# Optimization experiments

Measured on AMD Instinct MI355X. Metric: run time of the kernel, lower is better.

The kernel has to match this reference:

```python
import jax, jax.numpy as jnp
import numpy as np

BATCH, IN, OUT, G = 2048, 512, 512, 8


def setup_inputs() -> dict:
    key = jax.random.key(0)
    k1, k2, k3 = jax.random.split(key, 3)
    x = jax.random.normal(k1, (BATCH, IN), dtype=jnp.float32)
    # spline coefficients, initialized small like normal_(c, 0, 0.001)
    c = jax.random.normal(k2, (G, OUT, IN), dtype=jnp.float32) * 0.001
    # residual weights, xavier-like small init
    w_b = jax.random.normal(k3, (OUT, IN), dtype=jnp.float32) * 0.001
    w_s = jnp.ones((OUT, IN), dtype=jnp.float32)
    # RBF grid centers over [-2, 2] (get_size() == G)
    grid = jnp.arange(G, dtype=jnp.float32) * (4.0 / (G - 1)) - 2.0
    return {"x": x, "c": c, "w_b": w_b, "w_s": w_s, "grid": grid}


def _basis(x, grid):
    # Gaussian RBF basis: [batch, G, in]
    d = x[:, None, :] - grid[None, :, None]
    return jnp.exp(-(d * d))


def reference(x, c, w_b, w_s, grid):
    basis_vals = _basis(x, grid)                      # [b, n=G, i]
    # faithful to th.einsum('bni,aoi->boi', ...): n and a are independently summed
    spline_out = jnp.einsum('bni,aoi->boi', basis_vals, c)  # [b, o, i]
    spline_out = spline_out * w_s[None]
    res_out = jax.nn.silu(x)[:, None, :] * w_b[None]  # [b, o, i]
    return (spline_out + res_out).sum(axis=-1)        # [b, o]
```

## Files before the change

### kernel.cpp

```cpp
#include <hip/hip_runtime.h>

#define BATCH 2048
#define IN    512
#define OUT   512
#define NG    8
#define KTOT  1024

#define TILE_SHORTS 4096
#define NIT 16

typedef __attribute__((ext_vector_type(8))) short bf16x8;
typedef __attribute__((ext_vector_type(4))) float f32x4;

__device__ inline unsigned short f2bf(float f) {
    union { float f; unsigned int u; } v; v.f = f;
    unsigned int r = v.u + 0x7fffu + ((v.u >> 16) & 1u);
    return (unsigned short)(r >> 16);
}

__device__ inline void gload_lds16(const void* g, void* l) {
    __builtin_amdgcn_global_load_lds((const __attribute__((address_space(1))) void*)g,
                                     (__attribute__((address_space(3))) void*)l, 16, 0, 0);
}

__global__ __launch_bounds__(256) void prep_kernel(const float* __restrict__ x,
                                                   const float* __restrict__ c,
                                                   const float* __restrict__ w_b,
                                                   const float* __restrict__ w_s,
                                                   const float* __restrict__ grid,
                                                   unsigned short* __restrict__ A,
                                                   unsigned short* __restrict__ B) {
    int blk = blockIdx.x;
    int tid = threadIdx.x;
    if (blk < 512) {
        int e = (blk * 256 + tid) * 8;
        float g0 = grid[0];
        float dl = grid[1] - g0;
        float d2 = dl * dl;
        float dn[NG];
#pragma unroll
        for (int n = 0; n < NG; ++n) dn[n] = __expf(-d2 * (float)(n * n));
        float4 x0 = *(const float4*)&x[e];
        float4 x1 = *(const float4*)&x[e + 4];
        float xv[8] = {x0.x, x0.y, x0.z, x0.w, x1.x, x1.y, x1.z, x1.w};
        unsigned short sv[8], lv[8];
#pragma unroll
        for (int j = 0; j < 8; ++j) {
            float u  = xv[j] - g0;
            float e1 = __expf(-u * u);
            float q  = __expf(2.f * dl * u);
            float p  = dn[NG - 1];
#pragma unroll
            for (int n = NG - 2; n >= 0; --n) p = p * q + dn[n];
            sv[j] = f2bf(e1 * p);
            lv[j] = f2bf(xv[j] / (1.f + __expf(-xv[j])));
        }
        int b = e >> 9, i = e & 511;
        *(int4*)&A[b * KTOT + i]       = *(int4*)sv;
        *(int4*)&A[b * KTOT + 512 + i] = *(int4*)lv;
    } else {
        int e = ((blk - 512) * 256 + tid) * 8;
        float acc[8] = {};
#pragma unroll
        for (int a = 0; a < NG; ++a) {
            float4 c0 = *(const float4*)&c[(size_t)a * (OUT * IN) + e];
            float4 c1 = *(const float4*)&c[(size_t)a * (OUT * IN) + e + 4];
            acc[0] += c0.x; acc[1] += c0.y; acc[2] += c0.z; acc[3] += c0.w;
            acc[4] += c1.x; acc[5] += c1.y; acc[6] += c1.z; acc[7] += c1.w;
        }
        float4 s0 = *(const float4*)&w_s[e];
        float4 s1 = *(const float4*)&w_s[e + 4];
        float sw[8] = {s0.x, s0.y, s0.z, s0.w, s1.x, s1.y, s1.z, s1.w};
        float4 b0 = *(const float4*)&w_b[e];
        float4 b1 = *(const float4*)&w_b[e + 4];
        float bw[8] = {b0.x, b0.y, b0.z, b0.w, b1.x, b1.y, b1.z, b1.w};
        unsigned short cv[8], bv[8];
#pragma unroll
        for (int j = 0; j < 8; ++j) { cv[j] = f2bf(acc[j] * sw[j]); bv[j] = f2bf(bw[j]); }
        int o = e >> 9, i = e & 511;
        *(int4*)&B[o * KTOT + i]       = *(int4*)cv;
        *(int4*)&B[o * KTOT + 512 + i] = *(int4*)bv;
    }
}

__global__ __launch_bounds__(512) void gemm_kernel(const unsigned short* __restrict__ A,
                                                   const unsigned short* __restrict__ B,
                                                   float* __restrict__ outp) {
    __shared__ short As[3][TILE_SHORTS];
    __shared__ short Bs[3][TILE_SHORTS];

    int tid  = threadIdx.x;
    int lane = tid & 63;
    int w    = tid >> 6;
    int wm   = (w >> 2) & 1;
    int wn   = (w >> 1) & 1;
    int ks   = w & 1;
    int lr   = lane & 15, lg = lane >> 4;

    int bid  = blockIdx.x;
    int mg   = bid & 7;
    int rest = bid >> 3;
    int sub  = rest >> 3;
    int ncol = rest & 7;
    int mt   = mg * 4 + sub;
    int m0   = mt * 64;
    int n0   = ncol * 64;

    int srow = tid >> 3;
    int gsc  = (tid & 7) ^ (srow & 7);
    const unsigned short* a_src = A + (size_t)(m0 + srow) * KTOT + gsc * 8;
    const unsigned short* b_src = B + (size_t)(n0 + srow) * KTOT + gsc * 8;

    int swc  = ((ks * 4 + lg) ^ (lr & 7)) * 8;
    int ra0  = (wm * 32 + lr)      * 64 + swc;
    int ra1  = (wm * 32 + 16 + lr) * 64 + swc;
    int rb0  = (wn * 32 + lr)      * 64 + swc;
    int rb1  = (wn * 32 + 16 + lr) * 64 + swc;

    f32x4 acc00 = {0.f, 0.f, 0.f, 0.f};
    f32x4 acc01 = {0.f, 0.f, 0.f, 0.f};
    f32x4 acc10 = {0.f, 0.f, 0.f, 0.f};
    f32x4 acc11 = {0.f, 0.f, 0.f, 0.f};

#define STAGE(t, buf) do { \
        gload_lds16(a_src + (t) * 64, &As[buf][tid * 8]); \
        gload_lds16(b_src + (t) * 64, &Bs[buf][tid * 8]); \
    } while (0)

    STAGE(0, 0);
    STAGE(1, 1);
    asm volatile("s_waitcnt vmcnt(2)" ::: "memory");
    __builtin_amdgcn_s_barrier();
    __builtin_amdgcn_sched_barrier(0);

#pragma unroll
    for (int it = 0; it < NIT; ++it) {
        int cur = it % 3;
        if (it + 2 < NIT) STAGE(it + 2, (it + 2) % 3);
        bf16x8 a0 = *(const bf16x8*)&As[cur][ra0];
        bf16x8 a1 = *(const bf16x8*)&As[cur][ra1];
        bf16x8 b0 = *(const bf16x8*)&Bs[cur][rb0];
        bf16x8 b1 = *(const bf16x8*)&Bs[cur][rb1];
        acc00 = __builtin_amdgcn_mfma_f32_16x16x32_bf16(a0, b0, acc00, 0, 0, 0);
        acc01 = __builtin_amdgcn_mfma_f32_16x16x32_bf16(a0, b1, acc01, 0, 0, 0);
        acc10 = __builtin_amdgcn_mfma_f32_16x16x32_bf16(a1, b0, acc10, 0, 0, 0);
        acc11 = __builtin_amdgcn_mfma_f32_16x16x32_bf16(a1, b1, acc11, 0, 0, 0);
        if (it + 1 < NIT) {
            if (it + 2 < NIT) asm volatile("s_waitcnt vmcnt(2)" ::: "memory");
            else              asm volatile("s_waitcnt vmcnt(0)" ::: "memory");
            __builtin_amdgcn_s_barrier();
            __builtin_amdgcn_sched_barrier(0);
        }
    }
#undef STAGE

    __syncthreads();
    float* Ls = (float*)&As[0][0];
    int p = w >> 1;
    if (ks == 1) {
        *(f32x4*)&Ls[p * 1024 + lane * 16 + 0]  = acc00;
        *(f32x4*)&Ls[p * 1024 + lane * 16 + 4]  = acc01;
        *(f32x4*)&Ls[p * 1024 + lane * 16 + 8]  = acc10;
        *(f32x4*)&Ls[p * 1024 + lane * 16 + 12] = acc11;
    }
    __syncthreads();
    if (ks == 0) {
        f32x4 p00 = *(const f32x4*)&Ls[p * 1024 + lane * 16 + 0];
        f32x4 p01 = *(const f32x4*)&Ls[p * 1024 + lane * 16 + 4];
        f32x4 p10 = *(const f32x4*)&Ls[p * 1024 + lane * 16 + 8];
        f32x4 p11 = *(const f32x4*)&Ls[p * 1024 + lane * 16 + 12];
        int orow = m0 + wm * 32 + lg * 4;
        int ocol = n0 + wn * 32 + lr;
#pragma unroll
        for (int r = 0; r < 4; ++r) {
            outp[(size_t)(orow + r) * OUT + ocol]           = acc00[r] + p00[r];
            outp[(size_t)(orow + r) * OUT + ocol + 16]      = acc01[r] + p01[r];
            outp[(size_t)(orow + 16 + r) * OUT + ocol]      = acc10[r] + p10[r];
            outp[(size_t)(orow + 16 + r) * OUT + ocol + 16] = acc11[r] + p11[r];
        }
    }
}

extern "C" void kernel_launch(void* const* d_in, const int* in_sizes, int n_in,
                              void* d_out, int out_size, void* d_ws, size_t ws_size,
                              hipStream_t stream) {
    (void)in_sizes; (void)n_in; (void)out_size; (void)ws_size;
    const float* x    = (const float*)d_in[0];
    const float* c    = (const float*)d_in[1];
    const float* w_b  = (const float*)d_in[2];
    const float* w_s  = (const float*)d_in[3];
    const float* grid = (const float*)d_in[4];
    float* outp = (float*)d_out;

    unsigned short* A = (unsigned short*)d_ws;
    unsigned short* B = A + (size_t)BATCH * KTOT;

    prep_kernel<<<512 + 128, 256, 0, stream>>>(x, c, w_b, w_s, grid, A, B);
    gemm_kernel<<<256, 512, 0, stream>>>(A, B, outp);
}
```

Baseline: 18.40 us.

## Split GEMM K dimension across two blocks and add reduction kernel

Doubles the GEMM grid so each block processes only half of the K dimension (spline or residual half), writing partial sums to a workspace buffer. A new reduce kernel sums the two partials into the output. This aims to raise CU occupancy and shorten per-block serial latency, at the cost of extra global traffic for partials and an additional kernel launch.

```diff
diff --git a/kernel.cpp b/kernel.cpp
--- a/kernel.cpp
+++ b/kernel.cpp
@@ -7,7 +7,7 @@
 #define KTOT  1024
 
 #define TILE_SHORTS 4096
-#define NIT 16
+#define NITH 8
 
 typedef __attribute__((ext_vector_type(8))) short bf16x8;
 typedef __attribute__((ext_vector_type(4))) float f32x4;
@@ -83,9 +83,9 @@
     }
 }
 
-__global__ __launch_bounds__(512) void gemm_kernel(const unsigned short* __restrict__ A,
-                                                   const unsigned short* __restrict__ B,
-                                                   float* __restrict__ outp) {
+__global__ __launch_bounds__(512, 4) void gemm_kernel(const unsigned short* __restrict__ A,
+                                                      const unsigned short* __restrict__ B,
+                                                      float* __restrict__ P) {
     __shared__ short As[3][TILE_SHORTS];
     __shared__ short Bs[3][TILE_SHORTS];
 
@@ -97,9 +97,11 @@
     int ks   = w & 1;
     int lr   = lane & 15, lg = lane >> 4;
 
-    int bid  = blockIdx.x;
-    int mg   = bid & 7;
-    int rest = bid >> 3;
+    int bid   = blockIdx.x;
+    int tile  = bid & 255;
+    int khalf = bid >> 8;
+    int mg   = tile & 7;
+    int rest = tile >> 3;
     int sub  = rest >> 3;
     int ncol = rest & 7;
     int mt   = mg * 4 + sub;
@@ -108,8 +110,8 @@
 
     int srow = tid >> 3;
     int gsc  = (tid & 7) ^ (srow & 7);
-    const unsigned short* a_src = A + (size_t)(m0 + srow) * KTOT + gsc * 8;
-    const unsigned short* b_src = B + (size_t)(n0 + srow) * KTOT + gsc * 8;
+    const unsigned short* a_src = A + (size_t)(m0 + srow) * KTOT + khalf * 512 + gsc * 8;
+    const unsigned short* b_src = B + (size_t)(n0 + srow) * KTOT + khalf * 512 + gsc * 8;
 
     int swc  = ((ks * 4 + lg) ^ (lr & 7)) * 8;
     int ra0  = (wm * 32 + lr)      * 64 + swc;
@@ -134,9 +136,9 @@
     __builtin_amdgcn_sched_barrier(0);
 
 #pragma unroll
-    for (int it = 0; it < NIT; ++it) {
+    for (int it = 0; it < NITH; ++it) {
         int cur = it % 3;
-        if (it + 2 < NIT) STAGE(it + 2, (it + 2) % 3);
+        if (it + 2 < NITH) STAGE(it + 2, (it + 2) % 3);
         bf16x8 a0 = *(const bf16x8*)&As[cur][ra0];
         bf16x8 a1 = *(const bf16x8*)&As[cur][ra1];
         bf16x8 b0 = *(const bf16x8*)&Bs[cur][rb0];
@@ -145,9 +147,9 @@
         acc01 = __builtin_amdgcn_mfma_f32_16x16x32_bf16(a0, b1, acc01, 0, 0, 0);
         acc10 = __builtin_amdgcn_mfma_f32_16x16x32_bf16(a1, b0, acc10, 0, 0, 0);
         acc11 = __builtin_amdgcn_mfma_f32_16x16x32_bf16(a1, b1, acc11, 0, 0, 0);
-        if (it + 1 < NIT) {
-            if (it + 2 < NIT) asm volatile("s_waitcnt vmcnt(2)" ::: "memory");
-            else              asm volatile("s_waitcnt vmcnt(0)" ::: "memory");
+        if (it + 1 < NITH) {
+            if (it + 2 < NITH) asm volatile("s_waitcnt vmcnt(2)" ::: "memory");
+            else               asm volatile("s_waitcnt vmcnt(0)" ::: "memory");
             __builtin_amdgcn_s_barrier();
             __builtin_amdgcn_sched_barrier(0);
         }
@@ -169,16 +171,31 @@
         f32x4 p01 = *(const f32x4*)&Ls[p * 1024 + lane * 16 + 4];
         f32x4 p10 = *(const f32x4*)&Ls[p * 1024 + lane * 16 + 8];
         f32x4 p11 = *(const f32x4*)&Ls[p * 1024 + lane * 16 + 12];
+        float* Pq = P + (size_t)khalf * (BATCH * OUT);
         int orow = m0 + wm * 32 + lg * 4;
         int ocol = n0 + wn * 32 + lr;
 #pragma unroll
         for (int r = 0; r < 4; ++r) {
-            outp[(size_t)(orow + r) * OUT + ocol]           = acc00[r] + p00[r];
-            outp[(size_t)(orow + r) * OUT + ocol + 16]      = acc01[r] + p01[r];
-            outp[(size_t)(orow + 16 + r) * OUT + ocol]      = acc10[r] + p10[r];
-            outp[(size_t)(orow + 16 + r) * OUT + ocol + 16] = acc11[r] + p11[r];
-        }
-    }
+            Pq[(size_t)(orow + r) * OUT + ocol]           = acc00[r] + p00[r];
+            Pq[(size_t)(orow + r) * OUT + ocol + 16]      = acc01[r] + p01[r];
+            Pq[(size_t)(orow + 16 + r) * OUT + ocol]      = acc10[r] + p10[r];
+            Pq[(size_t)(orow + 16 + r) * OUT + ocol + 16] = acc11[r] + p11[r];
+        }
+    }
+}
+
+__global__ __launch_bounds__(256) void reduce_kernel(const float* __restrict__ P,
+                                                     float* __restrict__ outp) {
+    int i = (blockIdx.x * 256 + threadIdx.x) * 8;
+    const float* P1 = P + (size_t)BATCH * OUT;
+    float4 a0 = *(const float4*)&P[i];
+    float4 a1 = *(const float4*)&P[i + 4];
+    float4 b0 = *(const float4*)&P1[i];
+    float4 b1 = *(const float4*)&P1[i + 4];
+    float4 o0 = make_float4(a0.x + b0.x, a0.y + b0.y, a0.z + b0.z, a0.w + b0.w);
+    float4 o1 = make_float4(a1.x + b1.x, a1.y + b1.y, a1.z + b1.z, a1.w + b1.w);
+    *(float4*)&outp[i]     = o0;
+    *(float4*)&outp[i + 4] = o1;
 }
 
 extern "C" void kernel_launch(void* const* d_in, const int* in_sizes, int n_in,
@@ -194,7 +211,9 @@
 
     unsigned short* A = (unsigned short*)d_ws;
     unsigned short* B = A + (size_t)BATCH * KTOT;
+    float* P = (float*)((char*)d_ws + (8u << 20));
 
     prep_kernel<<<512 + 128, 256, 0, stream>>>(x, c, w_b, w_s, grid, A, B);
-    gemm_kernel<<<256, 512, 0, stream>>>(A, B, outp);
-}
+    gemm_kernel<<<512, 512, 0, stream>>>(A, B, P);
+    reduce_kernel<<<512, 256, 0, stream>>>(P, outp);
+}
```

Measured after the change: 22.46 us. +22.1%, slower.
